# Performance work log

Hardware: AMD Instinct MI355X
Metric: run time of the kernel (lower is better)

The kernel has to match this reference:

```python
import jax, jax.numpy as jnp
import numpy as np

B, N, D = 16, 2048, 1024
H, DH = 8, 64
I = H * DH            # 512
L = 64                # num_latents
DEPTH = 6
FF = 4 * D


def setup_inputs() -> dict:
    key = jax.random.key(0)
    ks = jax.random.split(key, 8)
    s = 0.02  # weight scale to keep activations well-conditioned
    return {
        "x": jax.random.normal(ks[0], (B, N, D), jnp.float32),
        "mask": jax.random.randint(ks[1], (B, N), 0, 2, jnp.int32),
        "latents": jax.random.normal(ks[2], (L, D), jnp.float32),
        "ln_m_w": jnp.ones((DEPTH, D), jnp.float32),
        "ln_m_b": jnp.zeros((DEPTH, D), jnp.float32),
        "ln_l_w": jnp.ones((DEPTH, D), jnp.float32),
        "ln_l_b": jnp.zeros((DEPTH, D), jnp.float32),
        "Wq": jax.random.normal(ks[3], (DEPTH, D, I), jnp.float32) * s,
        "Wkv": jax.random.normal(ks[4], (DEPTH, D, 2 * I), jnp.float32) * s,
        "Wo": jax.random.normal(ks[5], (DEPTH, I, D), jnp.float32) * s,
        "ff_ln_w": jnp.ones((DEPTH, D), jnp.float32),
        "ff_ln_b": jnp.zeros((DEPTH, D), jnp.float32),
        "W1": jax.random.normal(ks[6], (DEPTH, D, FF), jnp.float32) * s,
        "W2": jax.random.normal(ks[7], (DEPTH, FF, D), jnp.float32) * s,
        "norm_w": jnp.ones((D,), jnp.float32),
        "norm_b": jnp.zeros((D,), jnp.float32),
    }


def _ln(x, w, b, eps=1e-5):
    mu = x.mean(-1, keepdims=True)
    var = ((x - mu) ** 2).mean(-1, keepdims=True)
    return (x - mu) * jax.lax.rsqrt(var + eps) * w + b


def reference(x, mask, latents, ln_m_w, ln_m_b, ln_l_w, ln_l_b,
              Wq, Wkv, Wo, ff_ln_w, ff_ln_b, W1, W2, norm_w, norm_b):
    b, n, d = x.shape
    Lq = latents.shape[0]
    depth = Wq.shape[0]
    h = H
    dh = Wq.shape[-1] // h
    scale = dh ** -0.5

    x4 = x[:, None]  # b 1 n d  (t = 1 media frame)
    lat = jnp.broadcast_to(latents, (b, 1, Lq, d)).astype(x.dtype)
    # mask==1 means masked-out; latents (L zeros) are always attendable
    fmask = jnp.concatenate([mask, jnp.zeros((b, Lq), mask.dtype)], axis=-1)
    mbool = (fmask == 1)[:, None, None, None, :]  # b 1 1 1 S -> broadcast to b t h i S

    for i in range(depth):
        xn = _ln(x4, ln_m_w[i], ln_m_b[i])
        lnl = _ln(lat, ln_l_w[i], ln_l_b[i])
        q = (lnl @ Wq[i]).reshape(b, 1, Lq, h, dh)
        kv = jnp.concatenate([xn, lnl], axis=-2) @ Wkv[i]  # b 1 S 2I
        k, v = jnp.split(kv, 2, axis=-1)
        S = k.shape[-2]
        k = k.reshape(b, 1, S, h, dh)
        v = v.reshape(b, 1, S, h, dh)
        sim = jnp.einsum('btihd,btjhd->bthij', q, k) * scale
        sim = jnp.where(mbool, -jnp.inf, sim)
        sim = sim - jax.lax.stop_gradient(sim.max(axis=-1, keepdims=True))
        attn = jax.nn.softmax(sim, axis=-1)
        out = jnp.einsum('bthij,btjhd->btihd', attn, v).reshape(b, 1, Lq, h * dh)
        lat = out @ Wo[i] + lat
        hf = jax.nn.gelu(_ln(lat, ff_ln_w[i], ff_ln_b[i]) @ W1[i], approximate=False)
        lat = hf @ W2[i] + lat
    return _ln(lat, norm_w, norm_b)
```

## Files before the change

kernel.cpp:

```cpp
#include <hip/hip_runtime.h>

typedef unsigned short u16;
typedef unsigned int u32;
typedef __attribute__((ext_vector_type(8))) short short8;
typedef __attribute__((ext_vector_type(4))) float f4;

#define DEV static __device__ __forceinline__

constexpr int BB = 16, NN = 2048, DD = 1024, HH = 8, DHD = 64, II = 512, LL = 64, DEPTHC = 6, FFC = 4096;

DEV u16 f2bf(float f) {
  union { float f; u32 u; } v; v.f = f;
  u32 r = v.u + 0x7FFFu + ((v.u >> 16) & 1u);
  return (u16)(r >> 16);
}

typedef const u32 __attribute__((address_space(1)))* gas_p;
typedef u32 __attribute__((address_space(3)))* las_p;
DEV void gl_lds16(const void* g, void* l) {
  __builtin_amdgcn_global_load_lds((gas_p)g, (las_p)l, 16, 0, 0);
}

__global__ __launch_bounds__(256) void maskscan_k(const int* __restrict__ mask,
    int* __restrict__ idx, int* __restrict__ cnt) {
  int b = blockIdx.x, tid = threadIdx.x;
  int lane = tid & 63, wv = tid >> 6;
  const int* mrow = mask + (size_t)b * NN;
  int base = tid * 8;
  int keep[8]; int local = 0;
  #pragma unroll
  for (int j = 0; j < 8; j++) { keep[j] = (mrow[base + j] == 0); local += keep[j]; }
  int incl = local;
  #pragma unroll
  for (int off = 1; off < 64; off <<= 1) {
    int v = __shfl_up(incl, off, 64);
    if (lane >= off) incl += v;
  }
  __shared__ int wsum[4];
  if (lane == 63) wsum[wv] = incl;
  __syncthreads();
  int wbase = 0;
  for (int w = 0; w < wv; w++) wbase += wsum[w];
  int pos = wbase + incl - local;
  #pragma unroll
  for (int j = 0; j < 8; j++) if (keep[j]) idx[(size_t)b * NN + pos++] = base + j;
  if (tid == 255) cnt[b] = wbase + incl;
}

__global__ __launch_bounds__(256) void ln_gather_k(const float* __restrict__ x,
    const int* __restrict__ idx, const int* __restrict__ cnt, u16* __restrict__ xcomp) {
  int b = blockIdx.y, j = blockIdx.x, tid = threadIdx.x;
  int c = cnt[b];
  if (j >= ((c + 127) & ~127)) return;
  ushort4* orow = (ushort4*)(xcomp + ((size_t)b * NN + j) * DD);
  if (j >= c) { orow[tid] = make_ushort4(0, 0, 0, 0); return; }
  int src = idx[(size_t)b * NN + j];
  const float4* rp = (const float4*)(x + ((size_t)b * NN + src) * DD);
  float4 v = rp[tid];
  float s = v.x + v.y + v.z + v.w;
  float s2 = v.x*v.x + v.y*v.y + v.z*v.z + v.w*v.w;
  #pragma unroll
  for (int off = 32; off >= 1; off >>= 1) {
    s  += __shfl_xor(s, off, 64);
    s2 += __shfl_xor(s2, off, 64);
  }
  __shared__ float red[8];
  int wv = tid >> 6;
  if ((tid & 63) == 0) { red[wv] = s; red[4 + wv] = s2; }
  __syncthreads();
  s  = red[0] + red[1] + red[2] + red[3];
  s2 = red[4] + red[5] + red[6] + red[7];
  float mu = s * (1.f / DD);
  float var = s2 * (1.f / DD) - mu * mu;
  float rstd = rsqrtf(var + 1e-5f);
  orow[tid] = make_ushort4(f2bf((v.x - mu) * rstd), f2bf((v.y - mu) * rstd),
                           f2bf((v.z - mu) * rstd), f2bf((v.w - mu) * rstd));
}

template<bool OUTF32, bool AFFINE>
__global__ __launch_bounds__(256) void ln_rows_k(const float* __restrict__ in,
    const float* __restrict__ w, const float* __restrict__ bias, void* __restrict__ out) {
  int row = blockIdx.x;
  int tid = threadIdx.x;
  const float4* rp = (const float4*)(in + (size_t)row * DD);
  float4 x = rp[tid];
  float s = x.x + x.y + x.z + x.w;
  float s2 = x.x*x.x + x.y*x.y + x.z*x.z + x.w*x.w;
  #pragma unroll
  for (int off = 32; off >= 1; off >>= 1) {
    s  += __shfl_xor(s, off, 64);
    s2 += __shfl_xor(s2, off, 64);
  }
  __shared__ float red[8];
  int wv = tid >> 6;
  if ((tid & 63) == 0) { red[wv] = s; red[4 + wv] = s2; }
  __syncthreads();
  s  = red[0] + red[1] + red[2] + red[3];
  s2 = red[4] + red[5] + red[6] + red[7];
  float mu = s * (1.f / DD);
  float var = s2 * (1.f / DD) - mu * mu;
  float rstd = rsqrtf(var + 1e-5f);
  float y[4] = {x.x, x.y, x.z, x.w};
  int col = tid * 4;
  #pragma unroll
  for (int j = 0; j < 4; j++) {
    float v = (y[j] - mu) * rstd;
    if (AFFINE) v = v * w[col + j] + bias[col + j];
    y[j] = v;
  }
  if (OUTF32) {
    float4 o = {y[0], y[1], y[2], y[3]};
    ((float4*)out)[(size_t)row * (DD/4) + tid] = o;
  } else {
    ushort4 o = make_ushort4(f2bf(y[0]), f2bf(y[1]), f2bf(y[2]), f2bf(y[3]));
    ((ushort4*)out)[(size_t)row * (DD/4) + tid] = o;
  }
}

__global__ __launch_bounds__(256) void lat_init_k(const float* __restrict__ latents, float* __restrict__ lat) {
  int idx = blockIdx.x * 256 + threadIdx.x;
  ((float4*)lat)[idx] = ((const float4*)latents)[idx & (LL * DD / 4 - 1)];
}

__global__ void zero_k(float* __restrict__ p, int n) {
  int i = blockIdx.x * 256 + threadIdx.x;
  if (i < n) p[i] = 0.f;
}

__global__ void transpall_k(const float* __restrict__ Wq, const float* __restrict__ Wkv,
    const float* __restrict__ Wo, const float* __restrict__ W1, const float* __restrict__ W2,
    const float* __restrict__ lnw, const float* __restrict__ lnb,
    u16* __restrict__ WqkvT, u16* __restrict__ WkvTf, u16* __restrict__ WoT,
    u16* __restrict__ W1T, u16* __restrict__ W2T, float* __restrict__ biaskv) {
  __shared__ float t[32][33];
  __shared__ float bred[8][32];
  int id = blockIdx.x;
  const float* in; u16* o1; int R, C, c0, r0;
  bool iskv = false;
  if (id < 512)       { in = Wq;  R = 1024; C = 512;  int l = id;        c0 = (l % 16) * 32;  r0 = (l / 16) * 32;  o1 = WqkvT; }
  else if (id < 1536) { in = Wkv; R = 1024; C = 1024; int l = id - 512;  c0 = (l % 32) * 32;  r0 = (l / 32) * 32;  o1 = WqkvT + 512 * 1024; iskv = true; }
  else if (id < 2048) { in = Wo;  R = 512;  C = 1024; int l = id - 1536; c0 = (l % 32) * 32;  r0 = (l / 32) * 32;  o1 = WoT; }
  else if (id < 6144) { in = W1;  R = 1024; C = 4096; int l = id - 2048; c0 = (l % 128) * 32; r0 = (l / 128) * 32; o1 = W1T; }
  else                { in = W2;  R = 4096; C = 1024; int l = id - 6144; c0 = (l % 32) * 32;  r0 = (l / 32) * 32;  o1 = W2T; }
  int tx = threadIdx.x, ty = threadIdx.y;
  #pragma unroll
  for (int j = 0; j < 4; j++)
    t[ty + j*8][tx] = in[(size_t)(r0 + ty + j*8) * C + c0 + tx];
  __syncthreads();
  #pragma unroll
  for (int j = 0; j < 4; j++) {
    float v = t[tx][ty + j*8];
    o1[(size_t)(c0 + ty + j*8) * R + r0 + tx] = f2bf(v);
  }
  if (iskv) {
    float sc = lnw[r0 + tx];
    #pragma unroll
    for (int j = 0; j < 4; j++)
      WkvTf[(size_t)(c0 + ty + j*8) * 1024 + r0 + tx] = f2bf(t[tx][ty + j*8] * sc);
    float partial = 0.f;
    #pragma unroll
    for (int rr = 0; rr < 4; rr++)
      partial += lnb[r0 + ty + rr*8] * t[ty + rr*8][tx];
    bred[ty][tx] = partial;
    __syncthreads();
    if (ty == 0) {
      float sum = 0.f;
      #pragma unroll
      for (int w = 0; w < 8; w++) sum += bred[w][tx];
      atomicAdd(&biaskv[c0 + tx], sum);
    }
  }
}

template<int EPI, bool SWZ>
__global__ __launch_bounds__(256) void gemm_k(const u16* __restrict__ A, const u16* __restrict__ Bm,
    void* __restrict__ C, const float* __restrict__ bias, const int* __restrict__ cnt,
    int M, int N, int K) {
  __shared__ __align__(16) u16 As[128 * 32];
  __shared__ __align__(16) u16 Bs[128 * 32];
  int tid = threadIdx.x;
  int wv = tid >> 6, lane = tid & 63;
  int m0, n0;
  if (SWZ) {
    int id = blockIdx.x;
    int xg = id & 7, t = id >> 3;
    int mtile = xg * 32 + (t >> 3);
    n0 = (t & 7) * 128;
    int batch = mtile >> 4;
    int ml = (mtile & 15) * 128;
    if (ml >= cnt[batch]) return;
    m0 = batch * NN + ml;
  } else {
    m0 = blockIdx.y * 128; n0 = blockIdx.x * 128;
  }
  int srow = wv * 16 + (lane >> 2);
  int scol = (lane & 3) * 8;
  const u16* gA0 = A + (size_t)(m0 + srow) * K + scol;
  const u16* gA1 = A + (size_t)(m0 + 64 + srow) * K + scol;
  const u16* gB0 = Bm + (size_t)(n0 + srow) * K + scol;
  const u16* gB1 = Bm + (size_t)(n0 + 64 + srow) * K + scol;
  u16* lA0 = &As[srow * 32 + scol];
  u16* lA1 = &As[(64 + srow) * 32 + scol];
  u16* lB0 = &Bs[srow * 32 + scol];
  u16* lB1 = &Bs[(64 + srow) * 32 + scol];
  int wm = (wv & 1) * 64, wn = (wv >> 1) * 64;
  int fr = lane & 15, fq = (lane >> 4) * 8;
  f4 acc[4][4];
  #pragma unroll
  for (int mi = 0; mi < 4; mi++)
    #pragma unroll
    for (int ni = 0; ni < 4; ni++) acc[mi][ni] = f4{0.f, 0.f, 0.f, 0.f};

  for (int k0 = 0; k0 < K; k0 += 32) {
    gl_lds16(gA0 + k0, lA0);
    gl_lds16(gA1 + k0, lA1);
    gl_lds16(gB0 + k0, lB0);
    gl_lds16(gB1 + k0, lB1);
    __syncthreads();
    short8 af[4], bfr[4];
    #pragma unroll
    for (int mi = 0; mi < 4; mi++)
      af[mi] = *(const short8*)&As[(wm + mi*16 + fr) * 32 + fq];
    #pragma unroll
    for (int ni = 0; ni < 4; ni++)
      bfr[ni] = *(const short8*)&Bs[(wn + ni*16 + fr) * 32 + fq];
    #pragma unroll
    for (int mi = 0; mi < 4; mi++)
      #pragma unroll
      for (int ni = 0; ni < 4; ni++)
        acc[mi][ni] = __builtin_amdgcn_mfma_f32_16x16x32_bf16(af[mi], bfr[ni], acc[mi][ni], 0, 0, 0);
    __syncthreads();
  }
  int er = (lane >> 4) * 4;
  int ec = lane & 15;
  #pragma unroll
  for (int mi = 0; mi < 4; mi++) {
    #pragma unroll
    for (int ni = 0; ni < 4; ni++) {
      int col = n0 + wn + ni*16 + ec;
      #pragma unroll
      for (int r = 0; r < 4; r++) {
        int row = m0 + wm + mi*16 + er + r;
        float v = acc[mi][ni][r];
        if (EPI == 1) v += bias[col];
        if (EPI == 2) v = 0.5f * v * (1.f + erff(v * 0.70710678118654752f));
        ((u16*)C)[(size_t)row * N + col] = f2bf(v);
      }
    }
  }
}

__global__ __launch_bounds__(256) void gemmsk_k(const u16* __restrict__ A, const u16* __restrict__ Bm,
    float* __restrict__ C, int M, int N, int K, int Kc) {
  __shared__ __align__(16) u16 As[128 * 32];
  __shared__ __align__(16) u16 Bs[128 * 32];
  int tid = threadIdx.x;
  int wv = tid >> 6, lane = tid & 63;
  int m0 = blockIdx.y * 128, n0 = blockIdx.x * 128;
  int kb = blockIdx.z * Kc;
  int srow = wv * 16 + (lane >> 2);
  int scol = (lane & 3) * 8;
  const u16* gA0 = A + (size_t)(m0 + srow) * K + kb + scol;
  const u16* gA1 = A + (size_t)(m0 + 64 + srow) * K + kb + scol;
  const u16* gB0 = Bm + (size_t)(n0 + srow) * K + kb + scol;
  const u16* gB1 = Bm + (size_t)(n0 + 64 + srow) * K + kb + scol;
  u16* lA0 = &As[srow * 32 + scol];
  u16* lA1 = &As[(64 + srow) * 32 + scol];
  u16* lB0 = &Bs[srow * 32 + scol];
  u16* lB1 = &Bs[(64 + srow) * 32 + scol];
  int wm = (wv & 1) * 64, wn = (wv >> 1) * 64;
  int fr = lane & 15, fq = (lane >> 4) * 8;
  f4 acc[4][4];
  #pragma unroll
  for (int mi = 0; mi < 4; mi++)
    #pragma unroll
    for (int ni = 0; ni < 4; ni++) acc[mi][ni] = f4{0.f, 0.f, 0.f, 0.f};

  for (int k0 = 0; k0 < Kc; k0 += 32) {
    gl_lds16(gA0 + k0, lA0);
    gl_lds16(gA1 + k0, lA1);
    gl_lds16(gB0 + k0, lB0);
    gl_lds16(gB1 + k0, lB1);
    __syncthreads();
    short8 af[4], bfr[4];
    #pragma unroll
    for (int mi = 0; mi < 4; mi++)
      af[mi] = *(const short8*)&As[(wm + mi*16 + fr) * 32 + fq];
    #pragma unroll
    for (int ni = 0; ni < 4; ni++)
      bfr[ni] = *(const short8*)&Bs[(wn + ni*16 + fr) * 32 + fq];
    #pragma unroll
    for (int mi = 0; mi < 4; mi++)
      #pragma unroll
      for (int ni = 0; ni < 4; ni++)
        acc[mi][ni] = __builtin_amdgcn_mfma_f32_16x16x32_bf16(af[mi], bfr[ni], acc[mi][ni], 0, 0, 0);
    __syncthreads();
  }
  int er = (lane >> 4) * 4;
  int ec = lane & 15;
  #pragma unroll
  for (int mi = 0; mi < 4; mi++)
    #pragma unroll
    for (int ni = 0; ni < 4; ni++) {
      int col = n0 + wn + ni*16 + ec;
      #pragma unroll
      for (int r = 0; r < 4; r++) {
        int row = m0 + wm + mi*16 + er + r;
        atomicAdd(&C[(size_t)row * N + col], acc[mi][ni][r]);
      }
    }
}

__global__ __launch_bounds__(256) void gemm64_k(const u16* __restrict__ A, const u16* __restrict__ Bm,
    u16* __restrict__ C, int M, int N, int K) {
  __shared__ __align__(16) u16 As[64 * 32];
  __shared__ __align__(16) u16 Bs[64 * 32];
  int tid = threadIdx.x;
  int wv = tid >> 6, lane = tid & 63;
  int m0 = blockIdx.y * 64, n0 = blockIdx.x * 64;
  int srow = tid >> 2;
  int scol = (tid & 3) * 8;
  const u16* gA = A + (size_t)(m0 + srow) * K + scol;
  const u16* gB = Bm + (size_t)(n0 + srow) * K + scol;
  u16* lA = &As[srow * 32 + scol];
  u16* lB = &Bs[srow * 32 + scol];
  int wm = (wv & 1) * 32, wn = (wv >> 1) * 32;
  int fr = lane & 15, fq = (lane >> 4) * 8;
  f4 acc[2][2];
  #pragma unroll
  for (int mi = 0; mi < 2; mi++)
    #pragma unroll
    for (int ni = 0; ni < 2; ni++) acc[mi][ni] = f4{0.f, 0.f, 0.f, 0.f};

  for (int k0 = 0; k0 < K; k0 += 32) {
    gl_lds16(gA + k0, lA);
    gl_lds16(gB + k0, lB);
    __syncthreads();
    short8 af[2], bfr[2];
    #pragma unroll
    for (int mi = 0; mi < 2; mi++)
      af[mi] = *(const short8*)&As[(wm + mi*16 + fr) * 32 + fq];
    #pragma unroll
    for (int ni = 0; ni < 2; ni++)
      bfr[ni] = *(const short8*)&Bs[(wn + ni*16 + fr) * 32 + fq];
    #pragma unroll
    for (int mi = 0; mi < 2; mi++)
      #pragma unroll
      for (int ni = 0; ni < 2; ni++)
        acc[mi][ni] = __builtin_amdgcn_mfma_f32_16x16x32_bf16(af[mi], bfr[ni], acc[mi][ni], 0, 0, 0);
    __syncthreads();
  }
  int er = (lane >> 4) * 4;
  int ec = lane & 15;
  #pragma unroll
  for (int mi = 0; mi < 2; mi++)
    #pragma unroll
    for (int ni = 0; ni < 2; ni++) {
      int col = n0 + wn + ni*16 + ec;
      #pragma unroll
      for (int r = 0; r < 4; r++) {
        int row = m0 + wm + mi*16 + er + r;
        C[(size_t)row * N + col] = f2bf(acc[mi][ni][r]);
      }
    }
}

__global__ __launch_bounds__(256) void attn_k(const u16* __restrict__ qkv,
    const u16* __restrict__ kvx, const int* __restrict__ cnt, u16* __restrict__ out) {
  int b = blockIdx.x >> 3;
  int h = blockIdx.x & 7;
  int tid = threadIdx.x;
  int wv = tid >> 6, lane = tid & 63;
  int fr = lane & 15, fq8 = (lane >> 4) * 8;
  int c = cnt[b];
  int nt = (c + 63) >> 6;

  __shared__ __align__(16) u16 ks[64 * 88];
  __shared__ __align__(16) u16 vs[64 * 88];
  __shared__ __align__(16) u16 ps[4][16 * 88];
  __shared__ float smask[64];

  const u16* qp = qkv + (size_t)(b * LL + wv * 16 + fr) * 1536 + h * DHD;
  short8 aq0 = *(const short8*)(qp + fq8);
  short8 aq1 = *(const short8*)(qp + 32 + fq8);

  float m_i[4], l_i[4];
  f4 o[4];
  #pragma unroll
  for (int r = 0; r < 4; r++) { m_i[r] = -1e30f; l_i[r] = 0.f; }
  #pragma unroll
  for (int dt = 0; dt < 4; dt++) o[dt] = f4{0.f, 0.f, 0.f, 0.f};

  const float scale = 0.125f;

  for (int t = 0; t <= nt; t++) {
    bool isLat = (t == nt);
    const u16* src;
    int rs;
    if (isLat) { src = qkv + (size_t)(b * LL) * 1536 + 512 + h * DHD; rs = 1536; }
    else       { src = kvx + (size_t)(b * NN + t * 64) * 1024 + h * DHD; rs = 1024; }
    __syncthreads();
    #pragma unroll
    for (int it = 0; it < 2; it++) {
      int cid = it * 256 + tid;
      int kr = cid >> 3, c8 = (cid & 7) * 8;
      int4 kvv = *(const int4*)(src + (size_t)kr * rs + c8);
      *(int4*)&ks[kr * 88 + c8] = kvv;
      int4 vvv = *(const int4*)(src + 512 + (size_t)kr * rs + c8);
      const u16* ve = (const u16*)&vvv;
      #pragma unroll
      for (int j = 0; j < 8; j++) vs[(c8 + j) * 88 + kr] = ve[j];
    }
    if (tid < 64)
      smask[tid] = (isLat || (t * 64 + tid < c)) ? 0.f : -1e30f;
    __syncthreads();

    f4 sim[4];
    #pragma unroll
    for (int ct = 0; ct < 4; ct++) {
      short8 b0 = *(const short8*)&ks[(ct*16 + fr) * 88 + fq8];
      short8 b1 = *(const short8*)&ks[(ct*16 + fr) * 88 + 32 + fq8];
      f4 s = f4{0.f, 0.f, 0.f, 0.f};
      s = __builtin_amdgcn_mfma_f32_16x16x32_bf16(aq0, b0, s, 0, 0, 0);
      s = __builtin_amdgcn_mfma_f32_16x16x32_bf16(aq1, b1, s, 0, 0, 0);
      float mk = smask[ct*16 + fr];
      #pragma unroll
      for (int r = 0; r < 4; r++) s[r] = s[r] * scale + mk;
      sim[ct] = s;
    }
    float mnew[4], alpha[4], p[4][4];
    #pragma unroll
    for (int r = 0; r < 4; r++) {
      float mx = fmaxf(fmaxf(sim[0][r], sim[1][r]), fmaxf(sim[2][r], sim[3][r]));
      #pragma unroll
      for (int off = 8; off >= 1; off >>= 1) mx = fmaxf(mx, __shfl_xor(mx, off, 16));
      mnew[r] = fmaxf(m_i[r], mx);
      alpha[r] = __expf(m_i[r] - mnew[r]);
      m_i[r] = mnew[r];
      float ssum = 0.f;
      #pragma unroll
      for (int ct = 0; ct < 4; ct++) { float e = __expf(sim[ct][r] - mnew[r]); p[ct][r] = e; ssum += e; }
      #pragma unroll
      for (int off = 8; off >= 1; off >>= 1) ssum += __shfl_xor(ssum, off, 16);
      l_i[r] = l_i[r] * alpha[r] + ssum;
    }
    #pragma unroll
    for (int ct = 0; ct < 4; ct++)
      #pragma unroll
      for (int r = 0; r < 4; r++)
        ps[wv][((lane>>4)*4 + r) * 88 + ct*16 + fr] = f2bf(p[ct][r]);
    #pragma unroll
    for (int dt = 0; dt < 4; dt++)
      #pragma unroll
      for (int r = 0; r < 4; r++) o[dt][r] *= alpha[r];
    short8 pa0 = *(const short8*)&ps[wv][fr * 88 + fq8];
    short8 pa1 = *(const short8*)&ps[wv][fr * 88 + 32 + fq8];
    #pragma unroll
    for (int dt = 0; dt < 4; dt++) {
      short8 bv0 = *(const short8*)&vs[(dt*16 + fr) * 88 + fq8];
      short8 bv1 = *(const short8*)&vs[(dt*16 + fr) * 88 + 32 + fq8];
      o[dt] = __builtin_amdgcn_mfma_f32_16x16x32_bf16(pa0, bv0, o[dt], 0, 0, 0);
      o[dt] = __builtin_amdgcn_mfma_f32_16x16x32_bf16(pa1, bv1, o[dt], 0, 0, 0);
    }
  }
  #pragma unroll
  for (int dt = 0; dt < 4; dt++)
    #pragma unroll
    for (int r = 0; r < 4; r++) {
      int row = b * LL + wv * 16 + (lane>>4)*4 + r;
      int col = h * DHD + dt*16 + fr;
      out[(size_t)row * II + col] = f2bf(o[dt][r] / l_i[r]);
    }
}

extern "C" void kernel_launch(void* const* d_in, const int* in_sizes, int n_in,
                              void* d_out, int out_size, void* d_ws, size_t ws_size,
                              hipStream_t stream) {
  (void)in_sizes; (void)n_in; (void)out_size; (void)ws_size;
  const float* x       = (const float*)d_in[0];
  const int*   mask    = (const int*)d_in[1];
  const float* latents = (const float*)d_in[2];
  const float* ln_m_w  = (const float*)d_in[3];
  const float* ln_m_b  = (const float*)d_in[4];
  const float* ln_l_w  = (const float*)d_in[5];
  const float* ln_l_b  = (const float*)d_in[6];
  const float* Wq      = (const float*)d_in[7];
  const float* Wkv     = (const float*)d_in[8];
  const float* Wo      = (const float*)d_in[9];
  const float* ff_ln_w = (const float*)d_in[10];
  const float* ff_ln_b = (const float*)d_in[11];
  const float* W1      = (const float*)d_in[12];
  const float* W2      = (const float*)d_in[13];
  const float* norm_w  = (const float*)d_in[14];
  const float* norm_b  = (const float*)d_in[15];
  float* out = (float*)d_out;

  char* ws = (char*)d_ws;
  size_t off = 0;
  auto alloc = [&](size_t bytes) -> void* {
    void* p = ws + off; off += (bytes + 255) & ~(size_t)255; return p;
  };
  u16* xcomp = (u16*)alloc((size_t)32768 * 1024 * 2);
  u16* kvx   = (u16*)alloc((size_t)32768 * 1024 * 2);
  int* idxb  = (int*)alloc((size_t)32768 * 4);
  int* cnt   = (int*)alloc(64);
  float* lat = (float*)alloc((size_t)1024 * 1024 * 4);
  u16* lnl   = (u16*)alloc((size_t)1024 * 1024 * 2);
  u16* latn  = (u16*)alloc((size_t)1024 * 1024 * 2);
  u16* qkv   = (u16*)alloc((size_t)1024 * 1536 * 2);
  u16* aout  = (u16*)alloc((size_t)1024 * 512 * 2);
  u16* hf    = (u16*)alloc((size_t)1024 * 4096 * 2);
  u16* WqkvT = (u16*)alloc((size_t)1536 * 1024 * 2);
  u16* WkvTf = (u16*)alloc((size_t)1024 * 1024 * 2);
  u16* WoT   = (u16*)alloc((size_t)1024 * 512 * 2);
  u16* W1T   = (u16*)alloc((size_t)4096 * 1024 * 2);
  u16* W2T   = (u16*)alloc((size_t)1024 * 4096 * 2);
  float* biaskv_all = (float*)alloc(6144 * 4);

  maskscan_k<<<16, 256, 0, stream>>>(mask, idxb, cnt);
  ln_gather_k<<<dim3(2048, 16), 256, 0, stream>>>(x, idxb, cnt, xcomp);
  lat_init_k<<<1024, 256, 0, stream>>>(latents, lat);
  zero_k<<<24, 256, 0, stream>>>(biaskv_all, 6144);

  for (int i = 0; i < DEPTHC; i++) {
    transpall_k<<<10240, dim3(32, 8), 0, stream>>>(
        Wq + (size_t)i*1024*512, Wkv + (size_t)i*1024*1024, Wo + (size_t)i*512*1024,
        W1 + (size_t)i*1024*4096, W2 + (size_t)i*4096*1024,
        ln_m_w + i*1024, ln_m_b + i*1024,
        WqkvT, WkvTf, WoT, W1T, W2T, biaskv_all + i*1024);
    ln_rows_k<false, true><<<1024, 256, 0, stream>>>(lat, ln_l_w + i*1024, ln_l_b + i*1024, lnl);
    gemm64_k<<<dim3(24, 16), 256, 0, stream>>>(lnl, WqkvT, qkv, 1024, 1536, 1024);
    gemm_k<1, true><<<2048, 256, 0, stream>>>(xcomp, WkvTf, kvx, biaskv_all + i*1024, cnt, 32768, 1024, 1024);
    attn_k<<<128, 256, 0, stream>>>(qkv, kvx, cnt, aout);
    gemmsk_k<<<dim3(8, 8, 4), 256, 0, stream>>>(aout, WoT, lat, 1024, 1024, 512, 128);
    ln_rows_k<false, true><<<1024, 256, 0, stream>>>(lat, ff_ln_w + i*1024, ff_ln_b + i*1024, latn);
    gemm_k<2, false><<<dim3(32, 8), 256, 0, stream>>>(latn, W1T, hf, nullptr, nullptr, 1024, 4096, 1024);
    gemmsk_k<<<dim3(8, 8, 4), 256, 0, stream>>>(hf, W2T, lat, 1024, 1024, 4096, 1024);
  }
  ln_rows_k<true, true><<<1024, 256, 0, stream>>>(lat, norm_w, norm_b, out);
}
```

Measured before the change: 1.599 ms.

## Batch weight transposes, fuse QKV with KV GEMM, split attention over two halves

All six layers' weight transposes now run in one upfront launch into per-depth buffers, which removes six launches and the dependency stalls inside the loop. The small latent QKV GEMM moves into the same launch as the large masked KV GEMM, using 128x128 tiles, so both share one grid. Attention is split into two halves of the key tiles per (batch, head), giving 256 blocks instead of 128, and a small combine kernel merges the partial softmax results. The cost is more workspace memory, an extra combine launch, and fp32 partial results written to global memory.

```diff
diff --git a/kernel.cpp b/kernel.cpp
--- a/kernel.cpp
+++ b/kernel.cpp
@@ -77,7 +77,7 @@
                            f2bf((v.z - mu) * rstd), f2bf((v.w - mu) * rstd));
 }
 
-template<bool OUTF32, bool AFFINE>
+template<bool OUTF32>
 __global__ __launch_bounds__(256) void ln_rows_k(const float* __restrict__ in,
     const float* __restrict__ w, const float* __restrict__ bias, void* __restrict__ out) {
   int row = blockIdx.x;
@@ -103,11 +103,8 @@
   float y[4] = {x.x, x.y, x.z, x.w};
   int col = tid * 4;
   #pragma unroll
-  for (int j = 0; j < 4; j++) {
-    float v = (y[j] - mu) * rstd;
-    if (AFFINE) v = v * w[col + j] + bias[col + j];
-    y[j] = v;
-  }
+  for (int j = 0; j < 4; j++)
+    y[j] = (y[j] - mu) * rstd * w[col + j] + bias[col + j];
   if (OUTF32) {
     float4 o = {y[0], y[1], y[2], y[3]};
     ((float4*)out)[(size_t)row * (DD/4) + tid] = o;
@@ -127,32 +124,35 @@
   if (i < n) p[i] = 0.f;
 }
 
-__global__ void transpall_k(const float* __restrict__ Wq, const float* __restrict__ Wkv,
-    const float* __restrict__ Wo, const float* __restrict__ W1, const float* __restrict__ W2,
-    const float* __restrict__ lnw, const float* __restrict__ lnb,
-    u16* __restrict__ WqkvT, u16* __restrict__ WkvTf, u16* __restrict__ WoT,
-    u16* __restrict__ W1T, u16* __restrict__ W2T, float* __restrict__ biaskv) {
+__global__ void transpall_k(const float* __restrict__ WqA, const float* __restrict__ WkvA,
+    const float* __restrict__ WoA, const float* __restrict__ W1A, const float* __restrict__ W2A,
+    const float* __restrict__ lnwA, const float* __restrict__ lnbA,
+    u16* __restrict__ WqkvTA, u16* __restrict__ WkvTfA, u16* __restrict__ WoTA,
+    u16* __restrict__ W1TA, u16* __restrict__ W2TA, float* __restrict__ biaskvA) {
   __shared__ float t[32][33];
   __shared__ float bred[8][32];
-  int id = blockIdx.x;
+  int gid = blockIdx.x;
+  int depth = gid / 10240;
+  int id = gid % 10240;
   const float* in; u16* o1; int R, C, c0, r0;
   bool iskv = false;
-  if (id < 512)       { in = Wq;  R = 1024; C = 512;  int l = id;        c0 = (l % 16) * 32;  r0 = (l / 16) * 32;  o1 = WqkvT; }
-  else if (id < 1536) { in = Wkv; R = 1024; C = 1024; int l = id - 512;  c0 = (l % 32) * 32;  r0 = (l / 32) * 32;  o1 = WqkvT + 512 * 1024; iskv = true; }
-  else if (id < 2048) { in = Wo;  R = 512;  C = 1024; int l = id - 1536; c0 = (l % 32) * 32;  r0 = (l / 32) * 32;  o1 = WoT; }
-  else if (id < 6144) { in = W1;  R = 1024; C = 4096; int l = id - 2048; c0 = (l % 128) * 32; r0 = (l / 128) * 32; o1 = W1T; }
-  else                { in = W2;  R = 4096; C = 1024; int l = id - 6144; c0 = (l % 32) * 32;  r0 = (l / 32) * 32;  o1 = W2T; }
+  if (id < 512)       { in = WqA  + (size_t)depth*1024*512;  R = 1024; C = 512;  int l = id;        c0 = (l % 16) * 32;  r0 = (l / 16) * 32;  o1 = WqkvTA + (size_t)depth*1536*1024; }
+  else if (id < 1536) { in = WkvA + (size_t)depth*1024*1024; R = 1024; C = 1024; int l = id - 512;  c0 = (l % 32) * 32;  r0 = (l / 32) * 32;  o1 = WqkvTA + (size_t)depth*1536*1024 + 512*1024; iskv = true; }
+  else if (id < 2048) { in = WoA  + (size_t)depth*512*1024;  R = 512;  C = 1024; int l = id - 1536; c0 = (l % 32) * 32;  r0 = (l / 32) * 32;  o1 = WoTA + (size_t)depth*1024*512; }
+  else if (id < 6144) { in = W1A  + (size_t)depth*1024*4096; R = 1024; C = 4096; int l = id - 2048; c0 = (l % 128) * 32; r0 = (l / 128) * 32; o1 = W1TA + (size_t)depth*4096*1024; }
+  else                { in = W2A  + (size_t)depth*4096*1024; R = 4096; C = 1024; int l = id - 6144; c0 = (l % 32) * 32;  r0 = (l / 32) * 32;  o1 = W2TA + (size_t)depth*1024*4096; }
   int tx = threadIdx.x, ty = threadIdx.y;
   #pragma unroll
   for (int j = 0; j < 4; j++)
     t[ty + j*8][tx] = in[(size_t)(r0 + ty + j*8) * C + c0 + tx];
   __syncthreads();
   #pragma unroll
-  for (int j = 0; j < 4; j++) {
-    float v = t[tx][ty + j*8];
-    o1[(size_t)(c0 + ty + j*8) * R + r0 + tx] = f2bf(v);
-  }
+  for (int j = 0; j < 4; j++)
+    o1[(size_t)(c0 + ty + j*8) * R + r0 + tx] = f2bf(t[tx][ty + j*8]);
   if (iskv) {
+    const float* lnw = lnwA + depth * 1024;
+    const float* lnb = lnbA + depth * 1024;
+    u16* WkvTf = WkvTfA + (size_t)depth*1024*1024;
     float sc = lnw[r0 + tx];
     #pragma unroll
     for (int j = 0; j < 4; j++)
@@ -167,22 +167,23 @@
       float sum = 0.f;
       #pragma unroll
       for (int w = 0; w < 8; w++) sum += bred[w][tx];
-      atomicAdd(&biaskv[c0 + tx], sum);
-    }
-  }
-}
-
-template<int EPI, bool SWZ>
-__global__ __launch_bounds__(256) void gemm_k(const u16* __restrict__ A, const u16* __restrict__ Bm,
-    void* __restrict__ C, const float* __restrict__ bias, const int* __restrict__ cnt,
-    int M, int N, int K) {
+      atomicAdd(&biaskvA[depth*1024 + c0 + tx], sum);
+    }
+  }
+}
+
+__global__ __launch_bounds__(256) void gemm_fused_k(
+    const u16* __restrict__ xcomp, const u16* __restrict__ WkvTf, u16* __restrict__ kvx,
+    const float* __restrict__ bias, const int* __restrict__ cnt,
+    const u16* __restrict__ lnl, const u16* __restrict__ WqkvT, u16* __restrict__ qkv) {
   __shared__ __align__(16) u16 As[128 * 32];
   __shared__ __align__(16) u16 Bs[128 * 32];
+  int id = blockIdx.x;
   int tid = threadIdx.x;
   int wv = tid >> 6, lane = tid & 63;
+  const u16 *A, *B; u16* C; int N; bool dobias;
   int m0, n0;
-  if (SWZ) {
-    int id = blockIdx.x;
+  if (id < 2048) {
     int xg = id & 7, t = id >> 3;
     int mtile = xg * 32 + (t >> 3);
     n0 = (t & 7) * 128;
@@ -190,9 +191,75 @@
     int ml = (mtile & 15) * 128;
     if (ml >= cnt[batch]) return;
     m0 = batch * NN + ml;
+    A = xcomp; B = WkvTf; C = kvx; N = 1024; dobias = true;
   } else {
-    m0 = blockIdx.y * 128; n0 = blockIdx.x * 128;
-  }
+    int l = id - 2048;
+    m0 = (l / 12) * 128; n0 = (l % 12) * 128;
+    A = lnl; B = WqkvT; C = qkv; N = 1536; dobias = false;
+  }
+  const int K = 1024;
+  int srow = wv * 16 + (lane >> 2);
+  int scol = (lane & 3) * 8;
+  const u16* gA0 = A + (size_t)(m0 + srow) * K + scol;
+  const u16* gA1 = A + (size_t)(m0 + 64 + srow) * K + scol;
+  const u16* gB0 = B + (size_t)(n0 + srow) * K + scol;
+  const u16* gB1 = B + (size_t)(n0 + 64 + srow) * K + scol;
+  u16* lA0 = &As[srow * 32 + scol];
+  u16* lA1 = &As[(64 + srow) * 32 + scol];
+  u16* lB0 = &Bs[srow * 32 + scol];
+  u16* lB1 = &Bs[(64 + srow) * 32 + scol];
+  int wm = (wv & 1) * 64, wn = (wv >> 1) * 64;
+  int fr = lane & 15, fq = (lane >> 4) * 8;
+  f4 acc[4][4];
+  #pragma unroll
+  for (int mi = 0; mi < 4; mi++)
+    #pragma unroll
+    for (int ni = 0; ni < 4; ni++) acc[mi][ni] = f4{0.f, 0.f, 0.f, 0.f};
+
+  for (int k0 = 0; k0 < K; k0 += 32) {
+    gl_lds16(gA0 + k0, lA0);
+    gl_lds16(gA1 + k0, lA1);
+    gl_lds16(gB0 + k0, lB0);
+    gl_lds16(gB1 + k0, lB1);
+    __syncthreads();
+    short8 af[4], bfr[4];
+    #pragma unroll
+    for (int mi = 0; mi < 4; mi++)
+      af[mi] = *(const short8*)&As[(wm + mi*16 + fr) * 32 + fq];
+    #pragma unroll
+    for (int ni = 0; ni < 4; ni++)
+      bfr[ni] = *(const short8*)&Bs[(wn + ni*16 + fr) * 32 + fq];
+    #pragma unroll
+    for (int mi = 0; mi < 4; mi++)
+      #pragma unroll
+      for (int ni = 0; ni < 4; ni++)
+        acc[mi][ni] = __builtin_amdgcn_mfma_f32_16x16x32_bf16(af[mi], bfr[ni], acc[mi][ni], 0, 0, 0);
+    __syncthreads();
+  }
+  int er = (lane >> 4) * 4;
+  int ec = lane & 15;
+  #pragma unroll
+  for (int mi = 0; mi < 4; mi++) {
+    #pragma unroll
+    for (int ni = 0; ni < 4; ni++) {
+      int col = n0 + wn + ni*16 + ec;
+      float bv = dobias ? bias[col] : 0.f;
+      #pragma unroll
+      for (int r = 0; r < 4; r++) {
+        int row = m0 + wm + mi*16 + er + r;
+        C[(size_t)row * N + col] = f2bf(acc[mi][ni][r] + bv);
+      }
+    }
+  }
+}
+
+__global__ __launch_bounds__(256) void gemm_gelu_k(const u16* __restrict__ A, const u16* __restrict__ Bm,
+    u16* __restrict__ C, int M, int N, int K) {
+  __shared__ __align__(16) u16 As[128 * 32];
+  __shared__ __align__(16) u16 Bs[128 * 32];
+  int tid = threadIdx.x;
+  int wv = tid >> 6, lane = tid & 63;
+  int m0 = blockIdx.y * 128, n0 = blockIdx.x * 128;
   int srow = wv * 16 + (lane >> 2);
   int scol = (lane & 3) * 8;
   const u16* gA0 = A + (size_t)(m0 + srow) * K + scol;
@@ -234,7 +301,7 @@
   int er = (lane >> 4) * 4;
   int ec = lane & 15;
   #pragma unroll
-  for (int mi = 0; mi < 4; mi++) {
+  for (int mi = 0; mi < 4; mi++)
     #pragma unroll
     for (int ni = 0; ni < 4; ni++) {
       int col = n0 + wn + ni*16 + ec;
@@ -242,12 +309,10 @@
       for (int r = 0; r < 4; r++) {
         int row = m0 + wm + mi*16 + er + r;
         float v = acc[mi][ni][r];
-        if (EPI == 1) v += bias[col];
-        if (EPI == 2) v = 0.5f * v * (1.f + erff(v * 0.70710678118654752f));
-        ((u16*)C)[(size_t)row * N + col] = f2bf(v);
+        v = 0.5f * v * (1.f + erff(v * 0.70710678118654752f));
+        C[(size_t)row * N + col] = f2bf(v);
       }
     }
-  }
 }
 
 __global__ __launch_bounds__(256) void gemmsk_k(const u16* __restrict__ A, const u16* __restrict__ Bm,
@@ -311,69 +376,21 @@
     }
 }
 
-__global__ __launch_bounds__(256) void gemm64_k(const u16* __restrict__ A, const u16* __restrict__ Bm,
-    u16* __restrict__ C, int M, int N, int K) {
-  __shared__ __align__(16) u16 As[64 * 32];
-  __shared__ __align__(16) u16 Bs[64 * 32];
-  int tid = threadIdx.x;
-  int wv = tid >> 6, lane = tid & 63;
-  int m0 = blockIdx.y * 64, n0 = blockIdx.x * 64;
-  int srow = tid >> 2;
-  int scol = (tid & 3) * 8;
-  const u16* gA = A + (size_t)(m0 + srow) * K + scol;
-  const u16* gB = Bm + (size_t)(n0 + srow) * K + scol;
-  u16* lA = &As[srow * 32 + scol];
-  u16* lB = &Bs[srow * 32 + scol];
-  int wm = (wv & 1) * 32, wn = (wv >> 1) * 32;
-  int fr = lane & 15, fq = (lane >> 4) * 8;
-  f4 acc[2][2];
-  #pragma unroll
-  for (int mi = 0; mi < 2; mi++)
-    #pragma unroll
-    for (int ni = 0; ni < 2; ni++) acc[mi][ni] = f4{0.f, 0.f, 0.f, 0.f};
-
-  for (int k0 = 0; k0 < K; k0 += 32) {
-    gl_lds16(gA + k0, lA);
-    gl_lds16(gB + k0, lB);
-    __syncthreads();
-    short8 af[2], bfr[2];
-    #pragma unroll
-    for (int mi = 0; mi < 2; mi++)
-      af[mi] = *(const short8*)&As[(wm + mi*16 + fr) * 32 + fq];
-    #pragma unroll
-    for (int ni = 0; ni < 2; ni++)
-      bfr[ni] = *(const short8*)&Bs[(wn + ni*16 + fr) * 32 + fq];
-    #pragma unroll
-    for (int mi = 0; mi < 2; mi++)
-      #pragma unroll
-      for (int ni = 0; ni < 2; ni++)
-        acc[mi][ni] = __builtin_amdgcn_mfma_f32_16x16x32_bf16(af[mi], bfr[ni], acc[mi][ni], 0, 0, 0);
-    __syncthreads();
-  }
-  int er = (lane >> 4) * 4;
-  int ec = lane & 15;
-  #pragma unroll
-  for (int mi = 0; mi < 2; mi++)
-    #pragma unroll
-    for (int ni = 0; ni < 2; ni++) {
-      int col = n0 + wn + ni*16 + ec;
-      #pragma unroll
-      for (int r = 0; r < 4; r++) {
-        int row = m0 + wm + mi*16 + er + r;
-        C[(size_t)row * N + col] = f2bf(acc[mi][ni][r]);
-      }
-    }
-}
-
-__global__ __launch_bounds__(256) void attn_k(const u16* __restrict__ qkv,
-    const u16* __restrict__ kvx, const int* __restrict__ cnt, u16* __restrict__ out) {
-  int b = blockIdx.x >> 3;
-  int h = blockIdx.x & 7;
+__global__ __launch_bounds__(256) void attn_part_k(const u16* __restrict__ qkv,
+    const u16* __restrict__ kvx, const int* __restrict__ cnt,
+    float* __restrict__ opart, float* __restrict__ mlpart) {
+  int id = blockIdx.x;
+  int b = id >> 4;
+  int h = (id >> 1) & 7;
+  int half = id & 1;
   int tid = threadIdx.x;
   int wv = tid >> 6, lane = tid & 63;
   int fr = lane & 15, fq8 = (lane >> 4) * 8;
   int c = cnt[b];
   int nt = (c + 63) >> 6;
+  int T = nt + 1;
+  int t0 = half ? (T >> 1) : 0;
+  int t1 = half ? T : (T >> 1);
 
   __shared__ __align__(16) u16 ks[64 * 88];
   __shared__ __align__(16) u16 vs[64 * 88];
@@ -393,7 +410,7 @@
 
   const float scale = 0.125f;
 
-  for (int t = 0; t <= nt; t++) {
+  for (int t = t0; t < t1; t++) {
     bool isLat = (t == nt);
     const u16* src;
     int rs;
@@ -467,10 +484,44 @@
   for (int dt = 0; dt < 4; dt++)
     #pragma unroll
     for (int r = 0; r < 4; r++) {
-      int row = b * LL + wv * 16 + (lane>>4)*4 + r;
-      int col = h * DHD + dt*16 + fr;
-      out[(size_t)row * II + col] = f2bf(o[dt][r] / l_i[r]);
-    }
+      int row = wv * 16 + (lane>>4)*4 + r;
+      int col = dt*16 + fr;
+      opart[((size_t)id * 64 + row) * 64 + col] = o[dt][r];
+    }
+  if (fr == 0) {
+    #pragma unroll
+    for (int r = 0; r < 4; r++) {
+      int row = wv * 16 + (lane>>4)*4 + r;
+      mlpart[id * 128 + row * 2]     = m_i[r];
+      mlpart[id * 128 + row * 2 + 1] = l_i[r];
+    }
+  }
+}
+
+__global__ __launch_bounds__(256) void attn_comb_k(const float* __restrict__ opart,
+    const float* __restrict__ mlpart, u16* __restrict__ out) {
+  int bh = blockIdx.x;
+  int b = bh >> 3, h = bh & 7;
+  int id0 = bh * 2, id1 = bh * 2 + 1;
+  int tid = threadIdx.x;
+  int row = tid >> 2;
+  int c0 = (tid & 3) * 16;
+  float m0 = mlpart[id0 * 128 + row * 2], l0 = mlpart[id0 * 128 + row * 2 + 1];
+  float m1 = mlpart[id1 * 128 + row * 2], l1 = mlpart[id1 * 128 + row * 2 + 1];
+  float m = fmaxf(m0, m1);
+  float a0 = __expf(m0 - m), a1 = __expf(m1 - m);
+  float rl = 1.f / (l0 * a0 + l1 * a1);
+  const float4* p0 = (const float4*)(opart + ((size_t)id0 * 64 + row) * 64 + c0);
+  const float4* p1 = (const float4*)(opart + ((size_t)id1 * 64 + row) * 64 + c0);
+  u16* op = out + ((size_t)(b * LL + row)) * II + h * DHD + c0;
+  #pragma unroll
+  for (int j = 0; j < 4; j++) {
+    float4 v0 = p0[j], v1 = p1[j];
+    op[j*4 + 0] = f2bf((v0.x * a0 + v1.x * a1) * rl);
+    op[j*4 + 1] = f2bf((v0.y * a0 + v1.y * a1) * rl);
+    op[j*4 + 2] = f2bf((v0.z * a0 + v1.z * a1) * rl);
+    op[j*4 + 3] = f2bf((v0.w * a0 + v1.w * a1) * rl);
+  }
 }
 
 extern "C" void kernel_launch(void* const* d_in, const int* in_sizes, int n_in,
@@ -510,32 +561,34 @@
   u16* qkv   = (u16*)alloc((size_t)1024 * 1536 * 2);
   u16* aout  = (u16*)alloc((size_t)1024 * 512 * 2);
   u16* hf    = (u16*)alloc((size_t)1024 * 4096 * 2);
-  u16* WqkvT = (u16*)alloc((size_t)1536 * 1024 * 2);
-  u16* WkvTf = (u16*)alloc((size_t)1024 * 1024 * 2);
-  u16* WoT   = (u16*)alloc((size_t)1024 * 512 * 2);
-  u16* W1T   = (u16*)alloc((size_t)4096 * 1024 * 2);
-  u16* W2T   = (u16*)alloc((size_t)1024 * 4096 * 2);
-  float* biaskv_all = (float*)alloc(6144 * 4);
+  float* opart  = (float*)alloc((size_t)256 * 64 * 64 * 4);
+  float* mlpart = (float*)alloc((size_t)256 * 128 * 4);
+  u16* WqkvT = (u16*)alloc((size_t)DEPTHC * 1536 * 1024 * 2);
+  u16* WkvTf = (u16*)alloc((size_t)DEPTHC * 1024 * 1024 * 2);
+  u16* WoT   = (u16*)alloc((size_t)DEPTHC * 1024 * 512 * 2);
+  u16* W1T   = (u16*)alloc((size_t)DEPTHC * 4096 * 1024 * 2);
+  u16* W2T   = (u16*)alloc((size_t)DEPTHC * 1024 * 4096 * 2);
+  float* biaskv_all = (float*)alloc(DEPTHC * 1024 * 4);
 
   maskscan_k<<<16, 256, 0, stream>>>(mask, idxb, cnt);
   ln_gather_k<<<dim3(2048, 16), 256, 0, stream>>>(x, idxb, cnt, xcomp);
   lat_init_k<<<1024, 256, 0, stream>>>(latents, lat);
-  zero_k<<<24, 256, 0, stream>>>(biaskv_all, 6144);
+  zero_k<<<24, 256, 0, stream>>>(biaskv_all, DEPTHC * 1024);
+  transpall_k<<<DEPTHC * 10240, dim3(32, 8), 0, stream>>>(
+      Wq, Wkv, Wo, W1, W2, ln_m_w, ln_m_b,
+      WqkvT, WkvTf, WoT, W1T, W2T, biaskv_all);
 
   for (int i = 0; i < DEPTHC; i++) {
-    transpall_k<<<10240, dim3(32, 8), 0, stream>>>(
-        Wq + (size_t)i*1024*512, Wkv + (size_t)i*1024*1024, Wo + (size_t)i*512*1024,
-        W1 + (size_t)i*1024*4096, W2 + (size_t)i*4096*1024,
-        ln_m_w + i*1024, ln_m_b + i*1024,
-        WqkvT, WkvTf, WoT, W1T, W2T, biaskv_all + i*1024);
-    ln_rows_k<false, true><<<1024, 256, 0, stream>>>(lat, ln_l_w + i*1024, ln_l_b + i*1024, lnl);
-    gemm64_k<<<dim3(24, 16), 256, 0, stream>>>(lnl, WqkvT, qkv, 1024, 1536, 1024);
-    gemm_k<1, true><<<2048, 256, 0, stream>>>(xcomp, WkvTf, kvx, biaskv_all + i*1024, cnt, 32768, 1024, 1024);
-    attn_k<<<128, 256, 0, stream>>>(qkv, kvx, cnt, aout);
-    gemmsk_k<<<dim3(8, 8, 4), 256, 0, stream>>>(aout, WoT, lat, 1024, 1024, 512, 128);
-    ln_rows_k<false, true><<<1024, 256, 0, stream>>>(lat, ff_ln_w + i*1024, ff_ln_b + i*1024, latn);
-    gemm_k<2, false><<<dim3(32, 8), 256, 0, stream>>>(latn, W1T, hf, nullptr, nullptr, 1024, 4096, 1024);
-    gemmsk_k<<<dim3(8, 8, 4), 256, 0, stream>>>(hf, W2T, lat, 1024, 1024, 4096, 1024);
-  }
-  ln_rows_k<true, true><<<1024, 256, 0, stream>>>(lat, norm_w, norm_b, out);
-}
+    ln_rows_k<false><<<1024, 256, 0, stream>>>(lat, ln_l_w + i*1024, ln_l_b + i*1024, lnl);
+    gemm_fused_k<<<2144, 256, 0, stream>>>(
+        xcomp, WkvTf + (size_t)i*1024*1024, kvx, biaskv_all + i*1024, cnt,
+        lnl, WqkvT + (size_t)i*1536*1024, qkv);
+    attn_part_k<<<256, 256, 0, stream>>>(qkv, kvx, cnt, opart, mlpart);
+    attn_comb_k<<<128, 256, 0, stream>>>(opart, mlpart, aout);
+    gemmsk_k<<<dim3(8, 8, 4), 256, 0, stream>>>(aout, WoT + (size_t)i*1024*512, lat, 1024, 1024, 512, 128);
+    ln_rows_k<false><<<1024, 256, 0, stream>>>(lat, ff_ln_w + i*1024, ff_ln_b + i*1024, latn);
+    gemm_gelu_k<<<dim3(32, 8), 256, 0, stream>>>(latn, W1T + (size_t)i*4096*1024, hf, 1024, 4096, 1024);
+    gemmsk_k<<<dim3(8, 8, 4), 256, 0, stream>>>(hf, W2T + (size_t)i*1024*4096, lat, 1024, 1024, 4096, 1024);
+  }
+  ln_rows_k<true><<<1024, 256, 0, stream>>>(lat, norm_w, norm_b, out);
+}
```

New measurement: 1.497 ms. -6.4%, faster.
